# Optimization experiments

Hardware: AMD Instinct MI355X
Metric: run time of the kernel (lower is better)

Reference implementation:

```python
import jax, jax.numpy as jnp
import numpy as np

B, P, M, W = 32, 4096, 12, 9
IN_C, OUT_C = 64, 64
IN_PN_PAD = P + 1  # in_point_num + 1 padding row


def setup_inputs() -> dict:
    key = jax.random.key(0)
    k1, k2, k3, k4 = jax.random.split(key, 4)
    in_pc_pad = jax.random.normal(k1, (B, IN_PN_PAD, IN_C), dtype=jnp.float32)
    weights = jax.random.normal(k2, (W, OUT_C * IN_C), dtype=jnp.float32)
    bias = jnp.zeros((OUT_C,), dtype=jnp.float32)
    w_weights = jax.random.normal(k3, (P, M, W), dtype=jnp.float32) / (9.0 * W)
    neighbor_id_lstlst = jax.random.randint(k4, (P, M), 0, IN_PN_PAD, dtype=jnp.int64)
    neighbor_mask_lst = jnp.ones((P, M), dtype=jnp.float32)
    return {
        "in_pc_pad": in_pc_pad,
        "weights": weights,
        "bias": bias,
        "w_weights": w_weights,
        "neighbor_id_lstlst": neighbor_id_lstlst,
        "neighbor_mask_lst": neighbor_mask_lst,
    }


def reference(in_pc_pad, weights, bias, w_weights, neighbor_id_lstlst, neighbor_mask_lst):
    # gather neighbor features: [B, P, M, IN_C]
    in_neighbors = in_pc_pad[:, neighbor_id_lstlst]
    # mask the per-(point,neighbor) basis coefficients: [P, M, W]
    w2 = w_weights * neighbor_mask_lst[:, :, None]
    # synthesize per-(point,neighbor) weight matrices from basis: [P, M, OUT_C, IN_C]
    wmat = jnp.einsum('pmw,wc->pmc', w2, weights).reshape(P, M, OUT_C, IN_C)
    # batched matvec + neighbor-sum reduce (fused over m): [B, P, OUT_C]
    out_pc = jnp.einsum('pmoi,bpmi->bpo', wmat, in_neighbors)
    return out_pc + bias
```

## Files before the change

### kernel.cpp

```cpp
#include <hip/hip_runtime.h>
#include <hip/hip_bf16.h>

#define NB 32
#define NP 4096
#define NM 12
#define NW 9
#define NC 64
#define PN_PAD 4097
#define KDIM (NW * NC)
#define KSTEPS (KDIM / 32)
#define AROW 584

#define WSW_BYTES (KDIM * NC * 2)
#define W2_OFFSET WSW_BYTES
#define W2_BYTES (NP * NM * 12 * 4)
#define XB_OFFSET (W2_OFFSET + W2_BYTES)
#define XB_BYTES (NB * PN_PAD * NC * 2)
#define WS_NEED ((size_t)XB_OFFSET + XB_BYTES)

typedef __attribute__((ext_vector_type(8))) short short8;
typedef __attribute__((ext_vector_type(4))) float float4v;

__device__ __forceinline__ unsigned short f32_to_bf16(float f) {
    union { float f; unsigned u; } v; v.f = f;
    unsigned r = v.u + 0x7FFFu + ((v.u >> 16) & 1u);
    return (unsigned short)(r >> 16);
}

__device__ __forceinline__ uint2 pack_bf16x4(float4v v) {
    union { float f; unsigned u; } a0, a1, a2, a3;
    a0.f = v[0]; a1.f = v[1]; a2.f = v[2]; a3.f = v[3];
    unsigned u0 = a0.u + 0x8000u, u1 = a1.u + 0x8000u;
    unsigned u2 = a2.u + 0x8000u, u3 = a3.u + 0x8000u;
    uint2 r;
    r.x = __builtin_amdgcn_perm(u1, u0, 0x07060302u);
    r.y = __builtin_amdgcn_perm(u3, u2, 0x07060302u);
    return r;
}

__device__ __forceinline__ float4v bf16x4_to_f32(uint2 u) {
    union { unsigned u; float f; } c0, c1, c2, c3;
    c0.u = u.x << 16; c1.u = u.x & 0xFFFF0000u;
    c2.u = u.y << 16; c3.u = u.y & 0xFFFF0000u;
    return (float4v){c0.f, c1.f, c2.f, c3.f};
}

__global__ void prep(const float* __restrict__ w,
                     const float* __restrict__ ww,
                     const float* __restrict__ mask,
                     unsigned short* __restrict__ wsw,
                     float* __restrict__ w2d) {
    int idx = blockIdx.x * 256 + threadIdx.x;
    if (idx < KDIM * NC) {
        int j    = idx & 7;
        int lane = (idx >> 3) & 63;
        int nt   = (idx >> 9) & 3;
        int ks   = idx >> 11;
        int k = ks * 32 + ((lane >> 4) * 8) + j;
        int n = nt * 16 + (lane & 15);
        int wi = k >> 6;
        int ii = k & 63;
        wsw[idx] = f32_to_bf16(w[wi * (NC * NC) + n * NC + ii]);
    }
    if (idx < NP * NM * NW) {
        int wq = idx % NW;
        int pm = idx / NW;
        w2d[pm * 12 + wq] = ww[idx] * mask[pm];
    }
}

__global__ void prep_x(const float* __restrict__ x,
                       unsigned short* __restrict__ xb) {
    int idx = blockIdx.x * 256 + threadIdx.x;
    const int n4 = NB * PN_PAD * NC / 4;
    if (idx < n4) {
        const float4v* x4 = (const float4v*)x;
        ((uint2*)xb)[idx] = pack_bf16x4(x4[idx]);
    }
}

__global__ __launch_bounds__(512)
void conv_main_bf16(const float* __restrict__ x,
                    const unsigned short* __restrict__ xb,
                    const unsigned short* __restrict__ wsw,
                    const float* __restrict__ bias,
                    const float* __restrict__ w2d,
                    const int* __restrict__ nid,
                    float* __restrict__ out) {
    __shared__ __align__(16) unsigned short A[NB * AROW];

    const int p = blockIdx.x;
    const int tid = threadIdx.x;

    {
        const int i4 = tid & 15;
        const int b  = tid >> 4;
        const uint2* xb2 = (const uint2*)xb;
        const float* w2p = w2d + p * (NM * 12);
        const int* nidp = nid + p * NM;

        int nm[NM];
        #pragma unroll
        for (int m = 0; m < NM; ++m) nm[m] = nidp[m];

        uint2 xv[NM];
        #pragma unroll
        for (int m = 0; m < NM; ++m)
            xv[m] = xb2[(b * PN_PAD + nm[m]) * 16 + i4];

        float4v acc[NW];
        #pragma unroll
        for (int w = 0; w < NW; ++w) acc[w] = (float4v){0.f, 0.f, 0.f, 0.f};

        #pragma unroll
        for (int m = 0; m < NM; ++m) {
            const float4v xf = bf16x4_to_f32(xv[m]);
            #pragma unroll
            for (int w = 0; w < NW; ++w)
                acc[w] += w2p[m * 12 + w] * xf;
        }

        #pragma unroll
        for (int w = 0; w < NW; ++w)
            *(uint2*)&A[b * AROW + w * 64 + i4 * 4] = pack_bf16x4(acc[w]);
    }
    __syncthreads();

    {
        const int lane = tid & 63;
        const int wid  = tid >> 6;
        const int nt   = wid & 3;
        const int mt   = wid >> 2;
        const int quad = lane >> 4;
        const int l15  = lane & 15;

        float4v acc = {0.f, 0.f, 0.f, 0.f};
        const short8* Bfrags = (const short8*)wsw;
        const int arow = mt * 16 + l15;

        #pragma unroll
        for (int ks = 0; ks < KSTEPS; ++ks) {
            short8 bfrag = Bfrags[(ks * 4 + nt) * 64 + lane];
            const short8 a = *(const short8*)&A[arow * AROW + ks * 32 + quad * 8];
            acc = __builtin_amdgcn_mfma_f32_16x16x32_bf16(a, bfrag, acc, 0, 0, 0);
        }

        const int o = nt * 16 + l15;
        const float bv = bias[o];
        #pragma unroll
        for (int reg = 0; reg < 4; ++reg) {
            const int b = mt * 16 + quad * 4 + reg;
            out[(b * NP + p) * NC + o] = acc[reg] + bv;
        }
    }
}

__global__ __launch_bounds__(512)
void conv_main_fp32(const float* __restrict__ x,
                    const unsigned short* __restrict__ wsw,
                    const float* __restrict__ bias,
                    const float* __restrict__ w2d,
                    const int* __restrict__ nid,
                    float* __restrict__ out) {
    __shared__ __align__(16) unsigned short A[NB * AROW];
    const int p = blockIdx.x;
    const int tid = threadIdx.x;
    {
        const int i4 = tid & 15;
        const int b  = tid >> 4;
        const float4v* x4 = (const float4v*)x;
        const float* w2p = w2d + p * (NM * 12);
        const int* nidp = nid + p * NM;
        int nm[NM];
        #pragma unroll
        for (int m = 0; m < NM; ++m) nm[m] = nidp[m];
        float4v xv[NM];
        #pragma unroll
        for (int m = 0; m < NM; ++m)
            xv[m] = x4[(b * PN_PAD + nm[m]) * 16 + i4];
        float4v acc[NW];
        #pragma unroll
        for (int w = 0; w < NW; ++w) acc[w] = (float4v){0.f, 0.f, 0.f, 0.f};
        #pragma unroll
        for (int m = 0; m < NM; ++m) {
            #pragma unroll
            for (int w = 0; w < NW; ++w)
                acc[w] += w2p[m * 12 + w] * xv[m];
        }
        #pragma unroll
        for (int w = 0; w < NW; ++w)
            *(uint2*)&A[b * AROW + w * 64 + i4 * 4] = pack_bf16x4(acc[w]);
    }
    __syncthreads();
    {
        const int lane = tid & 63;
        const int wid  = tid >> 6;
        const int nt   = wid & 3;
        const int mt   = wid >> 2;
        const int quad = lane >> 4;
        const int l15  = lane & 15;
        float4v acc = {0.f, 0.f, 0.f, 0.f};
        const short8* Bfrags = (const short8*)wsw;
        const int arow = mt * 16 + l15;
        #pragma unroll
        for (int ks = 0; ks < KSTEPS; ++ks) {
            short8 bfrag = Bfrags[(ks * 4 + nt) * 64 + lane];
            const short8 a = *(const short8*)&A[arow * AROW + ks * 32 + quad * 8];
            acc = __builtin_amdgcn_mfma_f32_16x16x32_bf16(a, bfrag, acc, 0, 0, 0);
        }
        const int o = nt * 16 + l15;
        const float bv = bias[o];
        #pragma unroll
        for (int reg = 0; reg < 4; ++reg) {
            const int b = mt * 16 + quad * 4 + reg;
            out[(b * NP + p) * NC + o] = acc[reg] + bv;
        }
    }
}

extern "C" void kernel_launch(void* const* d_in, const int* in_sizes, int n_in,
                              void* d_out, int out_size, void* d_ws, size_t ws_size,
                              hipStream_t stream) {
    const float* x    = (const float*)d_in[0];
    const float* w    = (const float*)d_in[1];
    const float* bias = (const float*)d_in[2];
    const float* ww   = (const float*)d_in[3];
    const int*   nid  = (const int*)d_in[4];
    const float* mask = (const float*)d_in[5];
    float* out = (float*)d_out;
    unsigned short* wsw = (unsigned short*)d_ws;
    float* w2d = (float*)((char*)d_ws + W2_OFFSET);
    unsigned short* xb = (unsigned short*)((char*)d_ws + XB_OFFSET);

    const int prep_elems = NP * NM * NW;
    hipLaunchKernelGGL(prep, dim3((prep_elems + 255) / 256), dim3(256), 0, stream,
                       w, ww, mask, wsw, w2d);
    if (ws_size >= WS_NEED) {
        const int n4 = NB * PN_PAD * NC / 4;
        hipLaunchKernelGGL(prep_x, dim3((n4 + 255) / 256), dim3(256), 0, stream,
                           x, xb);
        hipLaunchKernelGGL(conv_main_bf16, dim3(NP), dim3(512), 0, stream,
                           x, xb, wsw, bias, w2d, nid, out);
    } else {
        hipLaunchKernelGGL(conv_main_fp32, dim3(NP), dim3(512), 0, stream,
                           x, wsw, bias, w2d, nid, out);
    }
}
```

Baseline: 136.6 us.

## Switch GEMM to 32x32x16 MFMA on two waves and fuse prep kernels

The weight fragment layout is rebuilt for the 32x32x16 bf16 MFMA, and the per-point GEMM now runs on 2 waves, each covering a 32x32 output tile, instead of 8 waves on 16x16 tiles. The two prep kernels are merged into a single templated launch, which removes one kernel launch. The neighbor accumulation is split into float2 halves so the compiler can use packed FMA. The aim is to cut launch overhead and raise MFMA efficiency, at the cost of leaving 6 of the 8 waves idle during the GEMM phase and writing outputs in a different access pattern.

```diff
diff --git a/kernel.cpp b/kernel.cpp
--- a/kernel.cpp
+++ b/kernel.cpp
@@ -1,5 +1,4 @@
 #include <hip/hip_runtime.h>
-#include <hip/hip_bf16.h>
 
 #define NB 32
 #define NP 4096
@@ -8,7 +7,7 @@
 #define NC 64
 #define PN_PAD 4097
 #define KDIM (NW * NC)
-#define KSTEPS (KDIM / 32)
+#define NKS (KDIM / 16)
 #define AROW 584
 
 #define WSW_BYTES (KDIM * NC * 2)
@@ -19,7 +18,9 @@
 #define WS_NEED ((size_t)XB_OFFSET + XB_BYTES)
 
 typedef __attribute__((ext_vector_type(8))) short short8;
+typedef __attribute__((ext_vector_type(2))) float float2v;
 typedef __attribute__((ext_vector_type(4))) float float4v;
+typedef __attribute__((ext_vector_type(16))) float float16v;
 
 __device__ __forceinline__ unsigned short f32_to_bf16(float f) {
     union { float f; unsigned u; } v; v.f = f;
@@ -38,26 +39,42 @@
     return r;
 }
 
-__device__ __forceinline__ float4v bf16x4_to_f32(uint2 u) {
+__device__ __forceinline__ uint2 pack_bf16x4_2(float2v lo, float2v hi) {
+    union { float f; unsigned u; } a0, a1, a2, a3;
+    a0.f = lo[0]; a1.f = lo[1]; a2.f = hi[0]; a3.f = hi[1];
+    unsigned u0 = a0.u + 0x8000u, u1 = a1.u + 0x8000u;
+    unsigned u2 = a2.u + 0x8000u, u3 = a3.u + 0x8000u;
+    uint2 r;
+    r.x = __builtin_amdgcn_perm(u1, u0, 0x07060302u);
+    r.y = __builtin_amdgcn_perm(u3, u2, 0x07060302u);
+    return r;
+}
+
+__device__ __forceinline__ void bf16x4_to_2xf2(uint2 u, float2v& lo, float2v& hi) {
     union { unsigned u; float f; } c0, c1, c2, c3;
     c0.u = u.x << 16; c1.u = u.x & 0xFFFF0000u;
     c2.u = u.y << 16; c3.u = u.y & 0xFFFF0000u;
-    return (float4v){c0.f, c1.f, c2.f, c3.f};
-}
-
-__global__ void prep(const float* __restrict__ w,
-                     const float* __restrict__ ww,
-                     const float* __restrict__ mask,
-                     unsigned short* __restrict__ wsw,
-                     float* __restrict__ w2d) {
+    lo = (float2v){c0.f, c1.f};
+    hi = (float2v){c2.f, c3.f};
+}
+
+template<int DOX>
+__global__ void prep_all(const float* __restrict__ w,
+                         const float* __restrict__ ww,
+                         const float* __restrict__ mask,
+                         const float* __restrict__ x,
+                         unsigned short* __restrict__ wsw,
+                         float* __restrict__ w2d,
+                         unsigned short* __restrict__ xb) {
     int idx = blockIdx.x * 256 + threadIdx.x;
     if (idx < KDIM * NC) {
         int j    = idx & 7;
         int lane = (idx >> 3) & 63;
-        int nt   = (idx >> 9) & 3;
-        int ks   = idx >> 11;
-        int k = ks * 32 + ((lane >> 4) * 8) + j;
-        int n = nt * 16 + (lane & 15);
+        int f    = idx >> 9;
+        int nt2  = f & 1;
+        int ks   = f >> 1;
+        int k = ks * 16 + ((lane >> 5) * 8) + j;
+        int n = nt2 * 32 + (lane & 31);
         int wi = k >> 6;
         int ii = k & 63;
         wsw[idx] = f32_to_bf16(w[wi * (NC * NC) + n * NC + ii]);
@@ -67,26 +84,24 @@
         int pm = idx / NW;
         w2d[pm * 12 + wq] = ww[idx] * mask[pm];
     }
-}
-
-__global__ void prep_x(const float* __restrict__ x,
-                       unsigned short* __restrict__ xb) {
-    int idx = blockIdx.x * 256 + threadIdx.x;
-    const int n4 = NB * PN_PAD * NC / 4;
-    if (idx < n4) {
-        const float4v* x4 = (const float4v*)x;
-        ((uint2*)xb)[idx] = pack_bf16x4(x4[idx]);
-    }
-}
-
+    if (DOX) {
+        const int n4 = NB * PN_PAD * NC / 4;
+        if (idx < n4) {
+            const float4v* x4 = (const float4v*)x;
+            ((uint2*)xb)[idx] = pack_bf16x4(x4[idx]);
+        }
+    }
+}
+
+template<int BF16X>
 __global__ __launch_bounds__(512)
-void conv_main_bf16(const float* __restrict__ x,
-                    const unsigned short* __restrict__ xb,
-                    const unsigned short* __restrict__ wsw,
-                    const float* __restrict__ bias,
-                    const float* __restrict__ w2d,
-                    const int* __restrict__ nid,
-                    float* __restrict__ out) {
+void conv_main(const float* __restrict__ x,
+               const unsigned short* __restrict__ xb,
+               const unsigned short* __restrict__ wsw,
+               const float* __restrict__ bias,
+               const float* __restrict__ w2d,
+               const int* __restrict__ nid,
+               float* __restrict__ out) {
     __shared__ __align__(16) unsigned short A[NB * AROW];
 
     const int p = blockIdx.x;
@@ -95,7 +110,6 @@
     {
         const int i4 = tid & 15;
         const int b  = tid >> 4;
-        const uint2* xb2 = (const uint2*)xb;
         const float* w2p = w2d + p * (NM * 12);
         const int* nidp = nid + p * NM;
 
@@ -103,117 +117,79 @@
         #pragma unroll
         for (int m = 0; m < NM; ++m) nm[m] = nidp[m];
 
-        uint2 xv[NM];
+        float2v acc0[NW], acc1[NW];
         #pragma unroll
-        for (int m = 0; m < NM; ++m)
-            xv[m] = xb2[(b * PN_PAD + nm[m]) * 16 + i4];
-
-        float4v acc[NW];
-        #pragma unroll
-        for (int w = 0; w < NW; ++w) acc[w] = (float4v){0.f, 0.f, 0.f, 0.f};
-
-        #pragma unroll
-        for (int m = 0; m < NM; ++m) {
-            const float4v xf = bf16x4_to_f32(xv[m]);
-            #pragma unroll
-            for (int w = 0; w < NW; ++w)
-                acc[w] += w2p[m * 12 + w] * xf;
+        for (int w = 0; w < NW; ++w) {
+            acc0[w] = (float2v){0.f, 0.f};
+            acc1[w] = (float2v){0.f, 0.f};
+        }
+
+        if (BF16X) {
+            const uint2* xb2 = (const uint2*)xb;
+            uint2 xv[NM];
+            #pragma unroll
+            for (int m = 0; m < NM; ++m)
+                xv[m] = xb2[(b * PN_PAD + nm[m]) * 16 + i4];
+            #pragma unroll
+            for (int m = 0; m < NM; ++m) {
+                float2v lo, hi;
+                bf16x4_to_2xf2(xv[m], lo, hi);
+                #pragma unroll
+                for (int w = 0; w < NW; ++w) {
+                    const float ws = w2p[m * 12 + w];
+                    acc0[w] += lo * ws;
+                    acc1[w] += hi * ws;
+                }
+            }
+        } else {
+            const float4v* x4 = (const float4v*)x;
+            float4v xv[NM];
+            #pragma unroll
+            for (int m = 0; m < NM; ++m)
+                xv[m] = x4[(b * PN_PAD + nm[m]) * 16 + i4];
+            #pragma unroll
+            for (int m = 0; m < NM; ++m) {
+                const float2v lo = {xv[m][0], xv[m][1]};
+                const float2v hi = {xv[m][2], xv[m][3]};
+                #pragma unroll
+                for (int w = 0; w < NW; ++w) {
+                    const float ws = w2p[m * 12 + w];
+                    acc0[w] += lo * ws;
+                    acc1[w] += hi * ws;
+                }
+            }
         }
 
         #pragma unroll
         for (int w = 0; w < NW; ++w)
-            *(uint2*)&A[b * AROW + w * 64 + i4 * 4] = pack_bf16x4(acc[w]);
+            *(uint2*)&A[b * AROW + w * 64 + i4 * 4] = pack_bf16x4_2(acc0[w], acc1[w]);
     }
     __syncthreads();
 
     {
         const int lane = tid & 63;
         const int wid  = tid >> 6;
-        const int nt   = wid & 3;
-        const int mt   = wid >> 2;
-        const int quad = lane >> 4;
-        const int l15  = lane & 15;
-
-        float4v acc = {0.f, 0.f, 0.f, 0.f};
-        const short8* Bfrags = (const short8*)wsw;
-        const int arow = mt * 16 + l15;
-
-        #pragma unroll
-        for (int ks = 0; ks < KSTEPS; ++ks) {
-            short8 bfrag = Bfrags[(ks * 4 + nt) * 64 + lane];
-            const short8 a = *(const short8*)&A[arow * AROW + ks * 32 + quad * 8];
-            acc = __builtin_amdgcn_mfma_f32_16x16x32_bf16(a, bfrag, acc, 0, 0, 0);
-        }
-
-        const int o = nt * 16 + l15;
-        const float bv = bias[o];
-        #pragma unroll
-        for (int reg = 0; reg < 4; ++reg) {
-            const int b = mt * 16 + quad * 4 + reg;
-            out[(b * NP + p) * NC + o] = acc[reg] + bv;
-        }
-    }
-}
-
-__global__ __launch_bounds__(512)
-void conv_main_fp32(const float* __restrict__ x,
-                    const unsigned short* __restrict__ wsw,
-                    const float* __restrict__ bias,
-                    const float* __restrict__ w2d,
-                    const int* __restrict__ nid,
-                    float* __restrict__ out) {
-    __shared__ __align__(16) unsigned short A[NB * AROW];
-    const int p = blockIdx.x;
-    const int tid = threadIdx.x;
-    {
-        const int i4 = tid & 15;
-        const int b  = tid >> 4;
-        const float4v* x4 = (const float4v*)x;
-        const float* w2p = w2d + p * (NM * 12);
-        const int* nidp = nid + p * NM;
-        int nm[NM];
-        #pragma unroll
-        for (int m = 0; m < NM; ++m) nm[m] = nidp[m];
-        float4v xv[NM];
-        #pragma unroll
-        for (int m = 0; m < NM; ++m)
-            xv[m] = x4[(b * PN_PAD + nm[m]) * 16 + i4];
-        float4v acc[NW];
-        #pragma unroll
-        for (int w = 0; w < NW; ++w) acc[w] = (float4v){0.f, 0.f, 0.f, 0.f};
-        #pragma unroll
-        for (int m = 0; m < NM; ++m) {
-            #pragma unroll
-            for (int w = 0; w < NW; ++w)
-                acc[w] += w2p[m * 12 + w] * xv[m];
-        }
-        #pragma unroll
-        for (int w = 0; w < NW; ++w)
-            *(uint2*)&A[b * AROW + w * 64 + i4 * 4] = pack_bf16x4(acc[w]);
-    }
-    __syncthreads();
-    {
-        const int lane = tid & 63;
-        const int wid  = tid >> 6;
-        const int nt   = wid & 3;
-        const int mt   = wid >> 2;
-        const int quad = lane >> 4;
-        const int l15  = lane & 15;
-        float4v acc = {0.f, 0.f, 0.f, 0.f};
-        const short8* Bfrags = (const short8*)wsw;
-        const int arow = mt * 16 + l15;
-        #pragma unroll
-        for (int ks = 0; ks < KSTEPS; ++ks) {
-            short8 bfrag = Bfrags[(ks * 4 + nt) * 64 + lane];
-            const short8 a = *(const short8*)&A[arow * AROW + ks * 32 + quad * 8];
-            acc = __builtin_amdgcn_mfma_f32_16x16x32_bf16(a, bfrag, acc, 0, 0, 0);
-        }
-        const int o = nt * 16 + l15;
-        const float bv = bias[o];
-        #pragma unroll
-        for (int reg = 0; reg < 4; ++reg) {
-            const int b = mt * 16 + quad * 4 + reg;
-            out[(b * NP + p) * NC + o] = acc[reg] + bv;
+        if (wid < 2) {
+            const int col  = lane & 31;
+            const int half = lane >> 5;
+            float16v acc = {0.f,0.f,0.f,0.f, 0.f,0.f,0.f,0.f,
+                            0.f,0.f,0.f,0.f, 0.f,0.f,0.f,0.f};
+            const short8* Bfrags = (const short8*)wsw;
+
+            #pragma unroll
+            for (int ks = 0; ks < NKS; ++ks) {
+                short8 bfrag = Bfrags[(ks * 2 + wid) * 64 + lane];
+                const short8 a = *(const short8*)&A[col * AROW + ks * 16 + half * 8];
+                acc = __builtin_amdgcn_mfma_f32_32x32x16_bf16(a, bfrag, acc, 0, 0, 0);
+            }
+
+            const int o = wid * 32 + col;
+            const float bv = bias[o];
+            #pragma unroll
+            for (int reg = 0; reg < 16; ++reg) {
+                const int b = (reg & 3) + 8 * (reg >> 2) + 4 * half;
+                out[(b * NP + p) * NC + o] = acc[reg] + bv;
+            }
         }
     }
 }
@@ -232,17 +208,17 @@
     float* w2d = (float*)((char*)d_ws + W2_OFFSET);
     unsigned short* xb = (unsigned short*)((char*)d_ws + XB_OFFSET);
 
-    const int prep_elems = NP * NM * NW;
-    hipLaunchKernelGGL(prep, dim3((prep_elems + 255) / 256), dim3(256), 0, stream,
-                       w, ww, mask, wsw, w2d);
     if (ws_size >= WS_NEED) {
         const int n4 = NB * PN_PAD * NC / 4;
-        hipLaunchKernelGGL(prep_x, dim3((n4 + 255) / 256), dim3(256), 0, stream,
-                           x, xb);
-        hipLaunchKernelGGL(conv_main_bf16, dim3(NP), dim3(512), 0, stream,
+        hipLaunchKernelGGL(prep_all<1>, dim3((n4 + 255) / 256), dim3(256), 0, stream,
+                           w, ww, mask, x, wsw, w2d, xb);
+        hipLaunchKernelGGL(conv_main<1>, dim3(NP), dim3(512), 0, stream,
                            x, xb, wsw, bias, w2d, nid, out);
     } else {
-        hipLaunchKernelGGL(conv_main_fp32, dim3(NP), dim3(512), 0, stream,
-                           x, wsw, bias, w2d, nid, out);
-    }
-}
+        const int prep_elems = NP * NM * NW;
+        hipLaunchKernelGGL(prep_all<0>, dim3((prep_elems + 255) / 256), dim3(256), 0, stream,
+                           w, ww, mask, x, wsw, w2d, xb);
+        hipLaunchKernelGGL(conv_main<0>, dim3(NP), dim3(512), 0, stream,
+                           x, xb, wsw, bias, w2d, nid, out);
+    }
+}
```

Result: faster. 131.0 us (-4.0%).
